# Performance work log

Measured on AMD Instinct MI355X. Metric: run time of the kernel, lower is better.

## Reference

```python
import jax, jax.numpy as jnp
import numpy as np

N = 100000
D = 256
E = 1600000
H, C = 2, 32  # heads, out_channels


def setup_inputs() -> dict:
    key = jax.random.key(0)
    ks = jax.random.split(key, 10)
    h_x = jax.random.normal(ks[0], (N, D), dtype=jnp.float32)
    t_x = jax.random.normal(ks[1], (N, D), dtype=jnp.float32)
    src = jax.random.randint(ks[2], (E,), 0, N, dtype=jnp.int32)
    off = jax.random.randint(ks[3], (E,), 1, N, dtype=jnp.int32)
    dst = (src + off) % N  # guarantees src != dst (remove_self_loops is a no-op)
    edge_index = jnp.stack([src, dst])  # [2, E]
    enrichment_weights = jax.random.uniform(ks[4], (E,), dtype=jnp.float32) * 3.0
    s = 1.0 / np.sqrt(D)
    W_src = jax.random.normal(ks[5], (D, H * C), dtype=jnp.float32) * s
    W_dst = jax.random.normal(ks[6], (D, H * C), dtype=jnp.float32) * s
    att_src = jax.random.normal(ks[7], (H, C), dtype=jnp.float32) * 0.1
    att_dst = jax.random.normal(ks[8], (H, C), dtype=jnp.float32) * 0.1
    bias = jnp.zeros((H * C,), dtype=jnp.float32)
    enrichment_scale = jnp.float32(0.5)
    return {"h_x": h_x, "t_x": t_x, "edge_index": edge_index,
            "enrichment_weights": enrichment_weights,
            "W_src": W_src, "W_dst": W_dst, "att_src": att_src,
            "att_dst": att_dst, "bias": bias,
            "enrichment_scale": enrichment_scale}


def _gat(x_src, x_dst, src, dst, num_dst, W_src, W_dst, att_src, att_dst, bias):
    # PyG GATConv, bipartite, heads=H, out=C, concat=True, eval mode
    hs = (x_src @ W_src).reshape(-1, H, C)  # [Ns, H, C]
    hd = (x_dst @ W_dst).reshape(-1, H, C)  # [Nd, H, C]
    a_s = jnp.einsum('nhc,hc->nh', hs, att_src)  # [Ns, H]
    a_d = jnp.einsum('nhc,hc->nh', hd, att_dst)  # [Nd, H]
    alpha = jax.nn.leaky_relu(a_s[src] + a_d[dst], 0.2)  # [E', H]
    m = jax.ops.segment_max(alpha, dst, num_segments=num_dst)
    alpha = jnp.exp(alpha - m[dst])
    z = jax.ops.segment_sum(alpha, dst, num_segments=num_dst)
    alpha = alpha / (z[dst] + 1e-16)
    msg = hs[src] * alpha[:, :, None]  # [E', H, C]
    out = jax.ops.segment_sum(msg, dst, num_segments=num_dst)  # [Nd, H, C]
    return out.reshape(num_dst, H * C) + bias


def reference(h_x, t_x, edge_index, enrichment_weights,
              W_src, W_dst, att_src, att_dst, bias, enrichment_scale):
    h_in = jax.nn.elu(h_x)
    t_in = jax.nn.elu(t_x)
    src, dst = edge_index[0], edge_index[1]
    loops = jnp.arange(min(h_x.shape[0], t_x.shape[0]), dtype=src.dtype)
    # direction 1: (h -> t), PyG appends self-loops after the input edges
    s1 = jnp.concatenate([src, loops]); d1 = jnp.concatenate([dst, loops])
    t_rep = _gat(h_in, t_in, s1, d1, t_x.shape[0], W_src, W_dst, att_src, att_dst, bias)
    # direction 2: reversed edges (t -> h)
    s2 = jnp.concatenate([dst, loops]); d2 = jnp.concatenate([src, loops])
    h_rep = _gat(t_in, h_in, s2, d2, h_x.shape[0], W_src, W_dst, att_src, att_dst, bias)
    # edge-enrichment reweighting (scalar factor)
    scale = 0.5 * jnp.tanh(enrichment_scale)
    ew = jnp.clip(enrichment_weights, 0.3, 3.0)
    aw = jax.nn.softmax(ew)
    weighted = jnp.sum(aw * ew)
    factor = 1.0 + scale * (weighted - 1.0)
    return (h_rep * factor, t_rep * factor)
```

## Files before the change

### kernel.cpp

```cpp
#include <hip/hip_runtime.h>
#include <hip/hip_fp16.h>
#include <math.h>

typedef __attribute__((ext_vector_type(8))) short bf16x8;
typedef __attribute__((ext_vector_type(4))) float f32x4;

__device__ __forceinline__ float bf2f(unsigned short u) {
    union { unsigned int i; float f; } c;
    c.i = ((unsigned int)u) << 16;
    return c.f;
}
__device__ __forceinline__ unsigned short f2bf(float f) {
    union { float f; unsigned int i; } c;
    c.f = f;
    unsigned int b = c.i + 0x7FFFu + ((c.i >> 16) & 1u);
    return (unsigned short)(b >> 16);
}
__device__ __forceinline__ float eluf(float v) {
    return v > 0.f ? v : (__expf(v) - 1.f);
}
__device__ __forceinline__ float lrelu(float v) {
    return v >= 0.f ? v : 0.2f * v;
}
__device__ __forceinline__ unsigned int fenc(float f) {
    union { float f; unsigned int u; } c; c.f = f;
    return (c.u & 0x80000000u) ? ~c.u : (c.u | 0x80000000u);
}
__device__ __forceinline__ float fdec(unsigned int k) {
    union { float f; unsigned int u; } c;
    c.u = (k & 0x80000000u) ? (k ^ 0x80000000u) : ~k;
    return c.f;
}

__global__ void detect_kernel(const unsigned int* __restrict__ w, int nwords,
                              int* __restrict__ flag)
{
    __shared__ int cnt_s;
    if (threadIdx.x == 0) cnt_s = 0;
    __syncthreads();
    int sane = 0;
    for (int i = threadIdx.x; i < nwords; i += 256) {
        unsigned int lo = w[i] & 0xffffu;
        int e = (int)((lo >> 7) & 0xffu);
        if (e >= 114 && e <= 136) sane++;
    }
    atomicAdd(&cnt_s, sane);
    __syncthreads();
    if (threadIdx.x == 0) *flag = (2 * cnt_s > nwords) ? 1 : 0;
}

__global__ __launch_bounds__(256) void wfrag_kernel(
    const void* __restrict__ Wsrc, const void* __restrict__ Wdst,
    const int* __restrict__ flag,
    unsigned short* __restrict__ Whi, unsigned short* __restrict__ Wlo)
{
    const int isbf = *flag;
    const int nch = 8 * 8 * 64;
    for (int ch = blockIdx.x * 256 + threadIdx.x; ch < nch; ch += gridDim.x * 256) {
        int l  = ch & 63;
        int t  = (ch >> 6) & 7;
        int ks = ch >> 9;
        int col = t * 16 + (l & 15);
        int k0  = ks * 32 + (l >> 4) * 8;
        if (isbf) {
            const unsigned short* W = (col < 64)
                ? ((const unsigned short*)Wsrc + col)
                : ((const unsigned short*)Wdst + (col - 64));
#pragma unroll
            for (int j = 0; j < 8; ++j) {
                Whi[(size_t)ch * 8 + j] = W[(size_t)(k0 + j) * 64];
                Wlo[(size_t)ch * 8 + j] = 0;
            }
        } else {
            const float* W = (col < 64)
                ? ((const float*)Wsrc + col)
                : ((const float*)Wdst + (col - 64));
#pragma unroll
            for (int j = 0; j < 8; ++j) {
                float wv = W[(size_t)(k0 + j) * 64];
                unsigned short h = f2bf(wv);
                Whi[(size_t)ch * 8 + j] = h;
                Wlo[(size_t)ch * 8 + j] = f2bf(wv - bf2f(h));
            }
        }
    }
}

__global__ __launch_bounds__(256) void gemm_fused_kernel(
    const void* __restrict__ xh, const void* __restrict__ xt,
    const unsigned short* __restrict__ Whi, const unsigned short* __restrict__ Wlo,
    const void* __restrict__ att_src, const void* __restrict__ att_dst,
    const int* __restrict__ flag,
    __half* __restrict__ P, float4* __restrict__ av, int N)
{
    const int isbf = *flag;
    __half* Pout = P + (size_t)blockIdx.y * (size_t)N * 64u;
    float4* avO  = av + (size_t)blockIdx.y * (size_t)N;
    const int tid = threadIdx.x;
    const int w   = tid >> 6;
    const int l   = tid & 63;
    const int l15 = l & 15;
    const int lhi = l >> 4;
    const int rowA = blockIdx.x * 64 + w * 16 + l15;
    const bool rv = rowA < N;

    bf16x8 ahi[8], alo[8];
    if (isbf) {
        const unsigned short* xv = (const unsigned short*)((blockIdx.y == 0) ? xh : xt);
#pragma unroll
        for (int ks = 0; ks < 8; ++ks) {
            union { bf16x8 v; unsigned int u[4]; } o;
            if (rv) {
                uint4 raw = *(const uint4*)(xv + (size_t)rowA * 256 + ks * 32 + lhi * 8);
                unsigned int wsr[4] = {raw.x, raw.y, raw.z, raw.w};
#pragma unroll
                for (int i = 0; i < 4; ++i) {
                    float lo = eluf(bf2f((unsigned short)(wsr[i] & 0xffffu)));
                    float hi = eluf(bf2f((unsigned short)(wsr[i] >> 16)));
                    o.u[i] = (unsigned int)f2bf(lo) | ((unsigned int)f2bf(hi) << 16);
                }
            } else {
                o.u[0] = o.u[1] = o.u[2] = o.u[3] = 0u;
            }
            ahi[ks] = o.v;
            alo[ks] = o.v;
        }
    } else {
        const float* xv = (const float*)((blockIdx.y == 0) ? xh : xt);
#pragma unroll
        for (int ks = 0; ks < 8; ++ks) {
            union { bf16x8 v; unsigned int u[4]; } oh, ol;
            if (rv) {
                const float4* px = (const float4*)(xv + (size_t)rowA * 256 + ks * 32 + lhi * 8);
                float4 f0 = px[0], f1 = px[1];
                float v[8] = {f0.x, f0.y, f0.z, f0.w, f1.x, f1.y, f1.z, f1.w};
#pragma unroll
                for (int i = 0; i < 8; ++i) v[i] = eluf(v[i]);
#pragma unroll
                for (int i = 0; i < 4; ++i) {
                    unsigned short h0 = f2bf(v[2 * i]);
                    unsigned short h1 = f2bf(v[2 * i + 1]);
                    unsigned short l0 = f2bf(v[2 * i]     - bf2f(h0));
                    unsigned short l1 = f2bf(v[2 * i + 1] - bf2f(h1));
                    oh.u[i] = (unsigned int)h0 | ((unsigned int)h1 << 16);
                    ol.u[i] = (unsigned int)l0 | ((unsigned int)l1 << 16);
                }
            } else {
                oh.u[0] = oh.u[1] = oh.u[2] = oh.u[3] = 0u;
                ol.u[0] = ol.u[1] = ol.u[2] = ol.u[3] = 0u;
            }
            ahi[ks] = oh.v;
            alo[ks] = ol.v;
        }
    }

    f32x4 acc[8];
#pragma unroll
    for (int t = 0; t < 8; ++t) acc[t] = (f32x4){0.f, 0.f, 0.f, 0.f};

    const bf16x8* wfh = (const bf16x8*)Whi;
    const bf16x8* wfl = (const bf16x8*)Wlo;
    if (isbf) {
#pragma unroll
        for (int ks = 0; ks < 8; ++ks) {
#pragma unroll
            for (int t = 0; t < 8; ++t) {
                bf16x8 b = wfh[(ks * 8 + t) * 64 + l];
                acc[t] = __builtin_amdgcn_mfma_f32_16x16x32_bf16(ahi[ks], b, acc[t], 0, 0, 0);
            }
        }
    } else {
#pragma unroll
        for (int ks = 0; ks < 8; ++ks) {
#pragma unroll
            for (int t = 0; t < 8; ++t) {
                bf16x8 bh = wfh[(ks * 8 + t) * 64 + l];
                bf16x8 bl = wfl[(ks * 8 + t) * 64 + l];
                acc[t] = __builtin_amdgcn_mfma_f32_16x16x32_bf16(ahi[ks], bh, acc[t], 0, 0, 0);
                acc[t] = __builtin_amdgcn_mfma_f32_16x16x32_bf16(alo[ks], bh, acc[t], 0, 0, 0);
                acc[t] = __builtin_amdgcn_mfma_f32_16x16x32_bf16(ahi[ks], bl, acc[t], 0, 0, 0);
            }
        }
    }

    float asv[4], adv[4];
#pragma unroll
    for (int t = 0; t < 4; ++t) {
        if (isbf) {
            asv[t] = bf2f(((const unsigned short*)att_src)[t * 16 + l15]);
            adv[t] = bf2f(((const unsigned short*)att_dst)[t * 16 + l15]);
        } else {
            asv[t] = ((const float*)att_src)[t * 16 + l15];
            adv[t] = ((const float*)att_dst)[t * 16 + l15];
        }
    }
    const int rbase = blockIdx.x * 64 + w * 16 + lhi * 4;
#pragma unroll
    for (int reg = 0; reg < 4; ++reg) {
        int row = rbase + reg;
        bool ok = row < N;
        if (ok) {
            __half* p = Pout + (size_t)row * 64 + l15;
#pragma unroll
            for (int t = 0; t < 4; ++t) p[t * 16] = __float2half(acc[t][reg]);
        }
        float s0 = acc[0][reg] * asv[0] + acc[1][reg] * asv[1];
        float s1 = acc[2][reg] * asv[2] + acc[3][reg] * asv[3];
        float d0 = acc[4][reg] * adv[0] + acc[5][reg] * adv[1];
        float d1 = acc[6][reg] * adv[2] + acc[7][reg] * adv[3];
#pragma unroll
        for (int o2 = 8; o2 >= 1; o2 >>= 1) {
            s0 += __shfl_xor(s0, o2, 64);
            s1 += __shfl_xor(s1, o2, 64);
            d0 += __shfl_xor(d0, o2, 64);
            d1 += __shfl_xor(d1, o2, 64);
        }
        if (ok && l15 == 0) avO[row] = make_float4(s0, s1, d0, d1);
    }
}

__global__ __launch_bounds__(256) void gemm_elu_kernel(
    const void* __restrict__ xh, const void* __restrict__ xt,
    const void* __restrict__ Wsrc, const void* __restrict__ Wdst,
    const void* __restrict__ att_src, const void* __restrict__ att_dst,
    const int* __restrict__ flag,
    __half* __restrict__ P, float4* __restrict__ av, int N, int D)
{
    const int isbf = *flag;
    __shared__ float xs[64][33];
    __shared__ float wt[32][128];
    const void* xv = (blockIdx.y == 0) ? xh : xt;
    __half* Pout = P + (size_t)blockIdx.y * (size_t)N * 64u;
    float4* avO  = av + (size_t)blockIdx.y * (size_t)N;
    const int rowBase = blockIdx.x * 64;
    const int tid = threadIdx.x;
    const int tcx = tid & 15;
    const int tcy = tid >> 4;

    float acc[4][8];
#pragma unroll
    for (int r = 0; r < 4; ++r)
#pragma unroll
        for (int c = 0; c < 8; ++c) acc[r][c] = 0.f;

    for (int kc = 0; kc < D; kc += 32) {
        {
            int row = tid >> 2;
            int kq  = (tid & 3) * 8;
            int r = rowBase + row;
            float v[8];
            if (r < N) {
                if (isbf) {
                    const unsigned short* xb = (const unsigned short*)xv;
                    uint4 raw = *(const uint4*)(xb + (size_t)r * D + kc + kq);
                    unsigned int ws[4] = {raw.x, raw.y, raw.z, raw.w};
#pragma unroll
                    for (int i = 0; i < 4; ++i) {
                        v[2 * i]     = bf2f((unsigned short)(ws[i] & 0xffffu));
                        v[2 * i + 1] = bf2f((unsigned short)(ws[i] >> 16));
                    }
                } else {
                    const float* xf = (const float*)xv;
                    const float4* p4 = (const float4*)(xf + (size_t)r * D + kc + kq);
                    float4 f0 = p4[0], f1 = p4[1];
                    v[0] = f0.x; v[1] = f0.y; v[2] = f0.z; v[3] = f0.w;
                    v[4] = f1.x; v[5] = f1.y; v[6] = f1.z; v[7] = f1.w;
                }
#pragma unroll
                for (int i = 0; i < 8; ++i) v[i] = eluf(v[i]);
            } else {
#pragma unroll
                for (int i = 0; i < 8; ++i) v[i] = 0.f;
            }
#pragma unroll
            for (int i = 0; i < 8; ++i) xs[row][kq + i] = v[i];
        }
#pragma unroll
        for (int i = 0; i < 2; ++i) {
            int f = (tid + i * 256) * 8;
            int k = f >> 7;
            int c = f & 127;
            float v[8];
            if (isbf) {
                const unsigned short* Wp = (c < 64)
                    ? ((const unsigned short*)Wsrc + (size_t)(kc + k) * 64 + c)
                    : ((const unsigned short*)Wdst + (size_t)(kc + k) * 64 + (c - 64));
                uint4 raw = *(const uint4*)Wp;
                unsigned int ws[4] = {raw.x, raw.y, raw.z, raw.w};
#pragma unroll
                for (int q = 0; q < 4; ++q) {
                    v[2 * q]     = bf2f((unsigned short)(ws[q] & 0xffffu));
                    v[2 * q + 1] = bf2f((unsigned short)(ws[q] >> 16));
                }
            } else {
                const float* Wp = (c < 64)
                    ? ((const float*)Wsrc + (size_t)(kc + k) * 64 + c)
                    : ((const float*)Wdst + (size_t)(kc + k) * 64 + (c - 64));
                const float4* p4 = (const float4*)Wp;
                float4 f0 = p4[0], f1 = p4[1];
                v[0] = f0.x; v[1] = f0.y; v[2] = f0.z; v[3] = f0.w;
                v[4] = f1.x; v[5] = f1.y; v[6] = f1.z; v[7] = f1.w;
            }
#pragma unroll
            for (int q = 0; q < 8; ++q) wt[k][c + q] = v[q];
        }
        __syncthreads();
#pragma unroll 8
        for (int k = 0; k < 32; ++k) {
            float xr[4];
#pragma unroll
            for (int r = 0; r < 4; ++r) xr[r] = xs[tcy * 4 + r][k];
            float4 w0 = *(const float4*)&wt[k][tcx * 8];
            float4 w1 = *(const float4*)&wt[k][tcx * 8 + 4];
#pragma unroll
            for (int r = 0; r < 4; ++r) {
                acc[r][0] += xr[r] * w0.x; acc[r][1] += xr[r] * w0.y;
                acc[r][2] += xr[r] * w0.z; acc[r][3] += xr[r] * w0.w;
                acc[r][4] += xr[r] * w1.x; acc[r][5] += xr[r] * w1.y;
                acc[r][6] += xr[r] * w1.z; acc[r][7] += xr[r] * w1.w;
            }
        }
        __syncthreads();
    }

    float attv[8];
#pragma unroll
    for (int q = 0; q < 8; ++q) {
        int c = tcx * 8 + q;
        if (isbf) attv[q] = (c < 64) ? bf2f(((const unsigned short*)att_src)[c])
                                     : bf2f(((const unsigned short*)att_dst)[c - 64]);
        else      attv[q] = (c < 64) ? ((const float*)att_src)[c]
                                     : ((const float*)att_dst)[c - 64];
    }

#pragma unroll
    for (int r = 0; r < 4; ++r) {
        int row = rowBase + tcy * 4 + r;
        bool ok = row < N;
        if (ok && tcx < 8) {
            __half* p = Pout + (size_t)row * 64 + tcx * 8;
#pragma unroll
            for (int q = 0; q < 8; ++q) p[q] = __float2half(acc[r][q]);
        }
        float part = 0.f;
#pragma unroll
        for (int q = 0; q < 8; ++q) part += acc[r][q] * attv[q];
        part += __shfl_xor(part, 1, 64);
        part += __shfl_xor(part, 2, 64);
        if (ok && (tcx & 3) == 0)
            ((float*)&avO[row])[tcx >> 2] = part;
    }
}

__global__ __launch_bounds__(256) void gmax_kernel(
    const float4* __restrict__ av, unsigned int* __restrict__ gmax, int N)
{
    unsigned int k0 = 0, k1 = 0, k2 = 0, k3 = 0;
    const int total = 2 * N;
    for (int i = blockIdx.x * 256 + threadIdx.x; i < total; i += gridDim.x * 256) {
        float4 v = av[i];
        unsigned int ex = fenc(v.x), ey = fenc(v.y);
        if (i < N) { k0 = max(k0, ex); k1 = max(k1, ey); }
        else       { k2 = max(k2, ex); k3 = max(k3, ey); }
    }
#pragma unroll
    for (int o = 32; o >= 1; o >>= 1) {
        k0 = max(k0, (unsigned int)__shfl_xor((int)k0, o, 64));
        k1 = max(k1, (unsigned int)__shfl_xor((int)k1, o, 64));
        k2 = max(k2, (unsigned int)__shfl_xor((int)k2, o, 64));
        k3 = max(k3, (unsigned int)__shfl_xor((int)k3, o, 64));
    }
    if ((threadIdx.x & 63) == 0) {
        atomicMax(&gmax[0], k0);
        atomicMax(&gmax[1], k1);
        atomicMax(&gmax[2], k2);
        atomicMax(&gmax[3], k3);
    }
}

__global__ void count_kernel(const int* __restrict__ srce, const int* __restrict__ dste,
                             int* __restrict__ cnt, int N, int E)
{
    int e = blockIdx.x * blockDim.x + threadIdx.x;
    if (e >= E) return;
    atomicAdd(&cnt[dste[e]], 1);
    atomicAdd(&cnt[N + srce[e]], 1);
}

__global__ __launch_bounds__(256) void scan_bsum_kernel(
    const int* __restrict__ cnt, int M, int chunk, int* __restrict__ bsum)
{
    __shared__ int r[4];
    int beg = blockIdx.x * chunk;
    int end = beg + chunk; if (end > M) end = M;
    int s = 0;
    for (int i = beg + threadIdx.x; i < end; i += 256) s += cnt[i];
#pragma unroll
    for (int o = 32; o >= 1; o >>= 1) s += __shfl_down(s, o, 64);
    int lane = threadIdx.x & 63, wv = threadIdx.x >> 6;
    if (lane == 0) r[wv] = s;
    __syncthreads();
    if (threadIdx.x == 0) bsum[blockIdx.x] = r[0] + r[1] + r[2] + r[3];
}

__global__ __launch_bounds__(256) void scan_boff_kernel(
    const int* __restrict__ bsum, int NB, int* __restrict__ boff)
{
    __shared__ int s[256];
    int t = threadIdx.x;
    int v = (t < NB) ? bsum[t] : 0;
    s[t] = v;
    __syncthreads();
    for (int o = 1; o < 256; o <<= 1) {
        int x = (t >= o) ? s[t - o] : 0;
        __syncthreads();
        s[t] += x;
        __syncthreads();
    }
    if (t < NB) boff[t] = s[t] - v;
}

__global__ __launch_bounds__(256) void scan_write_kernel(
    const int* __restrict__ cnt, int M, int chunk,
    const int* __restrict__ boff, int* __restrict__ off)
{
    __shared__ int s[256];
    int t = threadIdx.x;
    int beg = blockIdx.x * chunk;
    int end = beg + chunk; if (end > M) end = M;
    if (beg >= M) return;
    int running = boff[blockIdx.x];
    for (int base = beg; base < end; base += 256) {
        int i = base + t;
        int v = (i < end) ? cnt[i] : 0;
        s[t] = v;
        __syncthreads();
        for (int o = 1; o < 256; o <<= 1) {
            int x = (t >= o) ? s[t - o] : 0;
            __syncthreads();
            s[t] += x;
            __syncthreads();
        }
        if (i < end) off[i] = running + s[t] - v;
        int total = s[255];
        __syncthreads();
        running += total;
    }
    if (end == M && t == 0) off[M] = running;
}

__global__ void fill_kernel(const int* __restrict__ srce, const int* __restrict__ dste,
                            const int* __restrict__ off, int* __restrict__ cur,
                            const float4* __restrict__ av,
                            const unsigned int* __restrict__ gmax,
                            int4* __restrict__ epack, int N, int E)
{
    int e = blockIdx.x * blockDim.x + threadIdx.x;
    if (e >= E) return;
    int s = srce[e], d = dste[e];
    float4 ah = av[s];
    float4 at = av[N + d];
    float gm00 = fdec(gmax[0]), gm01 = fdec(gmax[1]);
    float gm10 = fdec(gmax[2]), gm11 = fdec(gmax[3]);
    float p00 = __expf(lrelu(ah.x + at.z) - lrelu(gm00 + at.z));
    float p01 = __expf(lrelu(ah.y + at.w) - lrelu(gm01 + at.w));
    float p10 = __expf(lrelu(at.x + ah.z) - lrelu(gm10 + ah.z));
    float p11 = __expf(lrelu(at.y + ah.w) - lrelu(gm11 + ah.w));
    int p  = atomicAdd(&cur[d], 1);
    epack[off[d] + p] = make_int4(s, __float_as_int(p00), __float_as_int(p01), 0);
    int p2 = atomicAdd(&cur[N + s], 1);
    epack[off[N + s] + p2] = make_int4(d, __float_as_int(p10), __float_as_int(p11), 0);
}

__global__ __launch_bounds__(256) void enrich_kernel(
    const void* __restrict__ ew, const int* __restrict__ flag,
    float* __restrict__ S, int E)
{
    __shared__ float r1[4], r2[4];
    const int isbf = *flag;
    float e1 = 0.f, e2 = 0.f;
    for (int i = blockIdx.x * 256 + threadIdx.x; i < E; i += gridDim.x * 256) {
        float c = isbf ? bf2f(((const unsigned short*)ew)[i]) : ((const float*)ew)[i];
        c = fminf(fmaxf(c, 0.3f), 3.0f);
        float ex = __expf(c);
        e1 += ex;
        e2 += c * ex;
    }
#pragma unroll
    for (int o = 32; o >= 1; o >>= 1) {
        e1 += __shfl_down(e1, o, 64);
        e2 += __shfl_down(e2, o, 64);
    }
    int lane = threadIdx.x & 63;
    int wv = threadIdx.x >> 6;
    if (lane == 0) { r1[wv] = e1; r2[wv] = e2; }
    __syncthreads();
    if (threadIdx.x == 0) {
        atomicAdd(&S[0], r1[0] + r1[1] + r1[2] + r1[3]);
        atomicAdd(&S[1], r2[0] + r2[1] + r2[2] + r2[3]);
    }
}

__global__ __launch_bounds__(256) void agg_kernel(
    const int* __restrict__ off, const int4* __restrict__ epack,
    const float4* __restrict__ av, const __half* __restrict__ Pall,
    const void* __restrict__ bias,
    const float* __restrict__ S,
    const unsigned int* __restrict__ gmax,
    const void* __restrict__ esc,
    const int* __restrict__ flag,
    void* __restrict__ out, int N)
{
    const int isbf = *flag;
    int q = (blockIdx.x * 256 + threadIdx.x) >> 6;
    int lane = threadIdx.x & 63;
    if (q >= 2 * N) return;
    int dir = (q >= N) ? 1 : 0;
    int n = q - dir * N;
    const __half* Psrc = Pall + (size_t)dir * (size_t)N * 64u;
    size_t outOff = dir ? 0u : (size_t)N * 64u;
    const int hi = lane >> 5;
    const int jb = off[q], je = off[q + 1];

    float4 asrc = av[(size_t)dir * N + n];
    float4 adst = av[(size_t)(1 - dir) * N + n];
    const float adv = hi ? adst.w : adst.z;
    const float m   = lrelu(fdec(gmax[dir * 2 + hi]) + adv);
    const float pSelf = __expf(lrelu((hi ? asrc.y : asrc.x) + adv) - m);

    float z0 = pSelf, z1 = 0.f, z2 = 0.f, z3 = 0.f;
    float a0 = pSelf * __half2float(Psrc[(size_t)n * 64 + lane]);
    float a1 = 0.f, a2 = 0.f, a3 = 0.f;

    int j = jb;
    for (; j + 3 < je; j += 4) {
        int4 e0 = epack[j], e1 = epack[j + 1], e2 = epack[j + 2], e3 = epack[j + 3];
        float h0 = __half2float(Psrc[(size_t)e0.x * 64 + lane]);
        float h1 = __half2float(Psrc[(size_t)e1.x * 64 + lane]);
        float h2 = __half2float(Psrc[(size_t)e2.x * 64 + lane]);
        float h3 = __half2float(Psrc[(size_t)e3.x * 64 + lane]);
        float p0 = __int_as_float(hi ? e0.z : e0.y);
        float p1 = __int_as_float(hi ? e1.z : e1.y);
        float p2 = __int_as_float(hi ? e2.z : e2.y);
        float p3 = __int_as_float(hi ? e3.z : e3.y);
        z0 += p0; a0 = fmaf(p0, h0, a0);
        z1 += p1; a1 = fmaf(p1, h1, a1);
        z2 += p2; a2 = fmaf(p2, h2, a2);
        z3 += p3; a3 = fmaf(p3, h3, a3);
    }
    for (; j < je; ++j) {
        int4 e0 = epack[j];
        float h0 = __half2float(Psrc[(size_t)e0.x * 64 + lane]);
        float p0 = __int_as_float(hi ? e0.z : e0.y);
        z0 += p0; a0 = fmaf(p0, h0, a0);
    }
    float z   = (z0 + z1) + (z2 + z3);
    float acc = (a0 + a1) + (a2 + a3);

    float escv = isbf ? bf2f(((const unsigned short*)esc)[0]) : ((const float*)esc)[0];
    float bv   = isbf ? bf2f(((const unsigned short*)bias)[lane]) : ((const float*)bias)[lane];
    float weighted = S[1] / S[0];
    float factor = 1.f + 0.5f * tanhf(escv) * (weighted - 1.f);
    float o = (acc / (z + 1e-16f) + bv) * factor;
    size_t oi = outOff + (size_t)n * 64 + lane;
    if (isbf) ((unsigned short*)out)[oi] = f2bf(o);
    else      ((float*)out)[oi] = o;
}

extern "C" void kernel_launch(void* const* d_in, const int* in_sizes, int n_in,
                              void* d_out, int out_size, void* d_ws, size_t ws_size,
                              hipStream_t stream)
{
    const void* hx      = d_in[0];
    const void* tx      = d_in[1];
    const int*  eidx    = (const int*)d_in[2];
    const void* ew      = d_in[3];
    const void* Wsrc    = d_in[4];
    const void* Wdst    = d_in[5];
    const void* att_src = d_in[6];
    const void* att_dst = d_in[7];
    const void* bias    = d_in[8];
    const void* esc     = d_in[9];

    const int HC = in_sizes[6];
    const int D  = in_sizes[4] / HC;
    const int N  = in_sizes[0] / D;
    const int E  = in_sizes[3];
    const int* srce = eidx;
    const int* dste = eidx + E;

    const bool canM = (D == 256) && (HC == 64);

    char* wsb = (char*)d_ws;
    size_t o = 0;
    auto alloc = [&](size_t bytes) -> void* {
        void* p = wsb + o;
        o += (bytes + 255) & ~(size_t)255;
        return p;
    };
    __half* Pall  = (__half*)alloc((size_t)2 * N * 64 * 2);
    float4* av    = (float4*)alloc((size_t)2 * N * 16);
    float* S      = (float*)alloc(2 * 4);
    unsigned int* gmax = (unsigned int*)alloc(4 * 4);
    int*   cnt    = (int*)alloc((size_t)2 * N * 4);
    int*   offp   = (int*)alloc(((size_t)2 * N + 1) * 4);
    int*   cur    = (int*)alloc((size_t)2 * N * 4);
    int4*  epack  = (int4*)alloc((size_t)2 * E * 16);
    int*   flag   = (int*)alloc(256);
    int*   bsum   = (int*)alloc(256 * 4);
    int*   boff   = (int*)alloc(256 * 4);
    unsigned short* Whi = (unsigned short*)alloc((size_t)8 * 8 * 64 * 8 * 2);
    unsigned short* Wlo = (unsigned short*)alloc((size_t)8 * 8 * 64 * 8 * 2);

    hipMemsetAsync(cnt, 0, (size_t)2 * N * 4, stream);
    hipMemsetAsync(cur, 0, (size_t)2 * N * 4, stream);
    hipMemsetAsync(S, 0, 2 * 4, stream);
    hipMemsetAsync(gmax, 0, 4 * 4, stream);

    detect_kernel<<<1, 256, 0, stream>>>((const unsigned int*)hx, 65536, flag);

    dim3 gGemm((N + 63) / 64, 2);
    if (canM) {
        wfrag_kernel<<<16, 256, 0, stream>>>(Wsrc, Wdst, flag, Whi, Wlo);
        gemm_fused_kernel<<<gGemm, 256, 0, stream>>>(hx, tx, Whi, Wlo,
                                                     att_src, att_dst, flag,
                                                     Pall, av, N);
    } else {
        gemm_elu_kernel<<<gGemm, 256, 0, stream>>>(hx, tx, Wsrc, Wdst, att_src, att_dst,
                                                   flag, Pall, av, N, D);
    }
    gmax_kernel<<<256, 256, 0, stream>>>(av, gmax, N);
    count_kernel<<<(E + 255) / 256, 256, 0, stream>>>(srce, dste, cnt, N, E);

    const int M = 2 * N;
    int chunk = (M + 255) / 256;
    chunk = (chunk + 255) & ~255;
    const int NB = (M + chunk - 1) / chunk;
    scan_bsum_kernel<<<NB, 256, 0, stream>>>(cnt, M, chunk, bsum);
    scan_boff_kernel<<<1, 256, 0, stream>>>(bsum, NB, boff);
    scan_write_kernel<<<NB, 256, 0, stream>>>(cnt, M, chunk, boff, offp);

    fill_kernel<<<(E + 255) / 256, 256, 0, stream>>>(srce, dste, offp, cur,
                                                     av, gmax, epack, N, E);
    enrich_kernel<<<512, 256, 0, stream>>>(ew, flag, S, E);

    agg_kernel<<<(2 * N + 3) / 4, 256, 0, stream>>>(offp, epack, av,
                                                    Pall, bias, S, gmax, esc, flag,
                                                    d_out, N);
}
```

Measured before the change: 884.0 us.

## Record CSR ranks during counting, pack edge weights as fp16, fuse enrichment reduction

The count kernel now keeps the rank returned by each atomicAdd, so fill no longer needs a second round of atomics on a cursor array or the memset that cleared it. The edge-weight reduction is folded into the count kernel, which removes the separate enrichment launch. Edge records shrink from 16 to 8 bytes by storing both heads' unnormalised attention weights as a packed half2, cutting write and gather traffic in fill and aggregation. In exchange it adds an E-sized rank buffer that is written and read back, and the attention weights lose precision from fp16 rounding.

Measured after the change: 874.4 us. Within noise of the previous version (-1.1%).

```diff
diff --git a/kernel.cpp b/kernel.cpp
--- a/kernel.cpp
+++ b/kernel.cpp
@@ -30,6 +30,11 @@
     union { float f; unsigned int u; } c;
     c.u = (k & 0x80000000u) ? (k ^ 0x80000000u) : ~k;
     return c.f;
+}
+__device__ __forceinline__ unsigned int packh2(float a, float b) {
+    __half2 h = __floats2half2_rn(a, b);
+    union { __half2 h; unsigned int u; } c; c.h = h;
+    return c.u;
 }
 
 __global__ void detect_kernel(const unsigned int* __restrict__ w, int nwords,
@@ -378,13 +383,40 @@
     }
 }
 
-__global__ void count_kernel(const int* __restrict__ srce, const int* __restrict__ dste,
-                             int* __restrict__ cnt, int N, int E)
-{
-    int e = blockIdx.x * blockDim.x + threadIdx.x;
-    if (e >= E) return;
-    atomicAdd(&cnt[dste[e]], 1);
-    atomicAdd(&cnt[N + srce[e]], 1);
+__global__ __launch_bounds__(256) void count_kernel(
+    const int* __restrict__ srce, const int* __restrict__ dste,
+    int* __restrict__ cnt, int2* __restrict__ rank,
+    const void* __restrict__ ew, const int* __restrict__ flag,
+    float* __restrict__ S, int N, int E)
+{
+    __shared__ float r1s[4], r2s[4];
+    const int isbf = *flag;
+    int e = blockIdx.x * 256 + threadIdx.x;
+    float e1 = 0.f, e2 = 0.f;
+    if (e < E) {
+        int s = srce[e], d = dste[e];
+        int r1 = atomicAdd(&cnt[d], 1);
+        int r2 = atomicAdd(&cnt[N + s], 1);
+        rank[e] = make_int2(r1, r2);
+        float c = isbf ? bf2f(((const unsigned short*)ew)[e]) : ((const float*)ew)[e];
+        c = fminf(fmaxf(c, 0.3f), 3.0f);
+        float ex = __expf(c);
+        e1 = ex;
+        e2 = c * ex;
+    }
+#pragma unroll
+    for (int o = 32; o >= 1; o >>= 1) {
+        e1 += __shfl_down(e1, o, 64);
+        e2 += __shfl_down(e2, o, 64);
+    }
+    int lane = threadIdx.x & 63;
+    int wv = threadIdx.x >> 6;
+    if (lane == 0) { r1s[wv] = e1; r2s[wv] = e2; }
+    __syncthreads();
+    if (threadIdx.x == 0) {
+        atomicAdd(&S[0], r1s[0] + r1s[1] + r1s[2] + r1s[3]);
+        atomicAdd(&S[1], r2s[0] + r2s[1] + r2s[2] + r2s[3]);
+    }
 }
 
 __global__ __launch_bounds__(256) void scan_bsum_kernel(
@@ -450,14 +482,15 @@
 }
 
 __global__ void fill_kernel(const int* __restrict__ srce, const int* __restrict__ dste,
-                            const int* __restrict__ off, int* __restrict__ cur,
+                            const int* __restrict__ off, const int2* __restrict__ rank,
                             const float4* __restrict__ av,
                             const unsigned int* __restrict__ gmax,
-                            int4* __restrict__ epack, int N, int E)
+                            int2* __restrict__ epack, int N, int E)
 {
     int e = blockIdx.x * blockDim.x + threadIdx.x;
     if (e >= E) return;
     int s = srce[e], d = dste[e];
+    int2 rk = rank[e];
     float4 ah = av[s];
     float4 at = av[N + d];
     float gm00 = fdec(gmax[0]), gm01 = fdec(gmax[1]);
@@ -466,43 +499,12 @@
     float p01 = __expf(lrelu(ah.y + at.w) - lrelu(gm01 + at.w));
     float p10 = __expf(lrelu(at.x + ah.z) - lrelu(gm10 + ah.z));
     float p11 = __expf(lrelu(at.y + ah.w) - lrelu(gm11 + ah.w));
-    int p  = atomicAdd(&cur[d], 1);
-    epack[off[d] + p] = make_int4(s, __float_as_int(p00), __float_as_int(p01), 0);
-    int p2 = atomicAdd(&cur[N + s], 1);
-    epack[off[N + s] + p2] = make_int4(d, __float_as_int(p10), __float_as_int(p11), 0);
-}
-
-__global__ __launch_bounds__(256) void enrich_kernel(
-    const void* __restrict__ ew, const int* __restrict__ flag,
-    float* __restrict__ S, int E)
-{
-    __shared__ float r1[4], r2[4];
-    const int isbf = *flag;
-    float e1 = 0.f, e2 = 0.f;
-    for (int i = blockIdx.x * 256 + threadIdx.x; i < E; i += gridDim.x * 256) {
-        float c = isbf ? bf2f(((const unsigned short*)ew)[i]) : ((const float*)ew)[i];
-        c = fminf(fmaxf(c, 0.3f), 3.0f);
-        float ex = __expf(c);
-        e1 += ex;
-        e2 += c * ex;
-    }
-#pragma unroll
-    for (int o = 32; o >= 1; o >>= 1) {
-        e1 += __shfl_down(e1, o, 64);
-        e2 += __shfl_down(e2, o, 64);
-    }
-    int lane = threadIdx.x & 63;
-    int wv = threadIdx.x >> 6;
-    if (lane == 0) { r1[wv] = e1; r2[wv] = e2; }
-    __syncthreads();
-    if (threadIdx.x == 0) {
-        atomicAdd(&S[0], r1[0] + r1[1] + r1[2] + r1[3]);
-        atomicAdd(&S[1], r2[0] + r2[1] + r2[2] + r2[3]);
-    }
+    epack[off[d] + rk.x]     = make_int2(s, (int)packh2(p00, p01));
+    epack[off[N + s] + rk.y] = make_int2(d, (int)packh2(p10, p11));
 }
 
 __global__ __launch_bounds__(256) void agg_kernel(
-    const int* __restrict__ off, const int4* __restrict__ epack,
+    const int* __restrict__ off, const int2* __restrict__ epack,
     const float4* __restrict__ av, const __half* __restrict__ Pall,
     const void* __restrict__ bias,
     const float* __restrict__ S,
@@ -520,6 +522,7 @@
     const __half* Psrc = Pall + (size_t)dir * (size_t)N * 64u;
     size_t outOff = dir ? 0u : (size_t)N * 64u;
     const int hi = lane >> 5;
+    const int sh = hi << 4;
     const int jb = off[q], je = off[q + 1];
 
     float4 asrc = av[(size_t)dir * N + n];
@@ -534,24 +537,24 @@
 
     int j = jb;
     for (; j + 3 < je; j += 4) {
-        int4 e0 = epack[j], e1 = epack[j + 1], e2 = epack[j + 2], e3 = epack[j + 3];
+        int2 e0 = epack[j], e1 = epack[j + 1], e2 = epack[j + 2], e3 = epack[j + 3];
         float h0 = __half2float(Psrc[(size_t)e0.x * 64 + lane]);
         float h1 = __half2float(Psrc[(size_t)e1.x * 64 + lane]);
         float h2 = __half2float(Psrc[(size_t)e2.x * 64 + lane]);
         float h3 = __half2float(Psrc[(size_t)e3.x * 64 + lane]);
-        float p0 = __int_as_float(hi ? e0.z : e0.y);
-        float p1 = __int_as_float(hi ? e1.z : e1.y);
-        float p2 = __int_as_float(hi ? e2.z : e2.y);
-        float p3 = __int_as_float(hi ? e3.z : e3.y);
+        float p0 = __half2float(__ushort_as_half((unsigned short)(((unsigned int)e0.y) >> sh)));
+        float p1 = __half2float(__ushort_as_half((unsigned short)(((unsigned int)e1.y) >> sh)));
+        float p2 = __half2float(__ushort_as_half((unsigned short)(((unsigned int)e2.y) >> sh)));
+        float p3 = __half2float(__ushort_as_half((unsigned short)(((unsigned int)e3.y) >> sh)));
         z0 += p0; a0 = fmaf(p0, h0, a0);
         z1 += p1; a1 = fmaf(p1, h1, a1);
         z2 += p2; a2 = fmaf(p2, h2, a2);
         z3 += p3; a3 = fmaf(p3, h3, a3);
     }
     for (; j < je; ++j) {
-        int4 e0 = epack[j];
+        int2 e0 = epack[j];
         float h0 = __half2float(Psrc[(size_t)e0.x * 64 + lane]);
-        float p0 = __int_as_float(hi ? e0.z : e0.y);
+        float p0 = __half2float(__ushort_as_half((unsigned short)(((unsigned int)e0.y) >> sh)));
         z0 += p0; a0 = fmaf(p0, h0, a0);
     }
     float z   = (z0 + z1) + (z2 + z3);
@@ -604,8 +607,8 @@
     unsigned int* gmax = (unsigned int*)alloc(4 * 4);
     int*   cnt    = (int*)alloc((size_t)2 * N * 4);
     int*   offp   = (int*)alloc(((size_t)2 * N + 1) * 4);
-    int*   cur    = (int*)alloc((size_t)2 * N * 4);
-    int4*  epack  = (int4*)alloc((size_t)2 * E * 16);
+    int2*  rank   = (int2*)alloc((size_t)E * 8);
+    int2*  epack  = (int2*)alloc((size_t)2 * E * 8);
     int*   flag   = (int*)alloc(256);
     int*   bsum   = (int*)alloc(256 * 4);
     int*   boff   = (int*)alloc(256 * 4);
@@ -613,7 +616,6 @@
     unsigned short* Wlo = (unsigned short*)alloc((size_t)8 * 8 * 64 * 8 * 2);
 
     hipMemsetAsync(cnt, 0, (size_t)2 * N * 4, stream);
-    hipMemsetAsync(cur, 0, (size_t)2 * N * 4, stream);
     hipMemsetAsync(S, 0, 2 * 4, stream);
     hipMemsetAsync(gmax, 0, 4 * 4, stream);
 
@@ -630,7 +632,8 @@
                                                    flag, Pall, av, N, D);
     }
     gmax_kernel<<<256, 256, 0, stream>>>(av, gmax, N);
-    count_kernel<<<(E + 255) / 256, 256, 0, stream>>>(srce, dste, cnt, N, E);
+    count_kernel<<<(E + 255) / 256, 256, 0, stream>>>(srce, dste, cnt, rank,
+                                                      ew, flag, S, N, E);
 
     const int M = 2 * N;
     int chunk = (M + 255) / 256;
@@ -640,9 +643,8 @@
     scan_boff_kernel<<<1, 256, 0, stream>>>(bsum, NB, boff);
     scan_write_kernel<<<NB, 256, 0, stream>>>(cnt, M, chunk, boff, offp);
 
-    fill_kernel<<<(E + 255) / 256, 256, 0, stream>>>(srce, dste, offp, cur,
+    fill_kernel<<<(E + 255) / 256, 256, 0, stream>>>(srce, dste, offp, rank,
                                                      av, gmax, epack, N, E);
-    enrich_kernel<<<512, 256, 0, stream>>>(ew, flag, S, E);
 
     agg_kernel<<<(2 * N + 3) / 4, 256, 0, stream>>>(offp, epack, av,
                                                     Pall, bias, S, gmax, esc, flag,
```
